# Kernel tuning notes

Measured on AMD Instinct MI355X. Metric: run time of the kernel, lower is better.

Reference implementation:

```python
import jax, jax.numpy as jnp
import numpy as np

N_SIDE = 32          # dense voxel grid side
WINDOW = 8           # window_size
C = 512              # channels
H = 8                # num_heads
D = C // H           # head_dim = 64
EPS = 1e-12          # torch F.normalize eps


def setup_inputs() -> dict:
    key = jax.random.key(0)
    ks = jax.random.split(key, 4)
    N = N_SIDE ** 3
    g = jnp.arange(N_SIDE, dtype=jnp.int32)
    zz, yy, xx = jnp.meshgrid(g, g, g, indexing='ij')
    # coords: [N, 4] = (batch_idx, x, y, z)
    coords = jnp.stack([jnp.zeros((N,), jnp.int32),
                        xx.reshape(-1), yy.reshape(-1), zz.reshape(-1)], axis=-1)
    x_feats = jax.random.normal(ks[0], (N, C), jnp.float32)
    w_qkv = jax.random.normal(ks[1], (C, 3 * C), jnp.float32) / np.sqrt(C).astype(np.float32)
    b_qkv = jnp.zeros((3 * C,), jnp.float32)
    gamma_q = jnp.ones((H, D), jnp.float32)
    gamma_k = jnp.ones((H, D), jnp.float32)
    w_out = jax.random.normal(ks[2], (C, C), jnp.float32) / np.sqrt(C).astype(np.float32)
    b_out = jnp.zeros((C,), jnp.float32)
    return dict(x_feats=x_feats, coords=coords, w_qkv=w_qkv, b_qkv=b_qkv,
                gamma_q=gamma_q, gamma_k=gamma_k, w_out=w_out, b_out=b_out)


def _mh_rms_norm(x, gamma):
    # SparseMultiHeadRMSNorm: L2-normalize last dim, scale by gamma * sqrt(dim)
    xf = x.astype(jnp.float32)
    norm = jnp.maximum(jnp.linalg.norm(xf, axis=-1, keepdims=True), EPS)
    return ((xf / norm) * gamma * np.float32(np.sqrt(D))).astype(x.dtype)


def reference(x_feats, coords, w_qkv, b_qkv, gamma_q, gamma_k, w_out, b_out):
    N = x_feats.shape[0]
    qkv = (x_feats @ w_qkv + b_qkv).reshape(N, 3, H, D)  # [N,3,H,D]
    q = _mh_rms_norm(qkv[:, 0], gamma_q)
    k = _mh_rms_norm(qkv[:, 1], gamma_k)
    v = qkv[:, 2]
    # windowed grouping: window id from voxel coords (shift_window = (0,0,0))
    wc = coords[:, 1:] // WINDOW                       # [N,3]
    nwin = N_SIDE // WINDOW
    wid = (wc[:, 0] * nwin + wc[:, 1]) * nwin + wc[:, 2]
    order = jnp.argsort(wid, stable=True)              # gather points into windows
    inv = jnp.argsort(order)                           # scatter back
    M = WINDOW ** 3                                    # points per window (dense grid)
    W = N // M                                         # number of windows
    qg = q[order].reshape(W, M, H, D)
    kg = k[order].reshape(W, M, H, D)
    vg = v[order].reshape(W, M, H, D)
    scores = jnp.einsum('wmhd,wnhd->whmn', qg, kg) / np.float32(np.sqrt(D))
    attn = jax.nn.softmax(scores, axis=-1)
    hg = jnp.einsum('whmn,wnhd->wmhd', attn, vg)       # [W,M,H,D]
    h = hg.reshape(W * M, H * D)[inv]                  # back to original point order
    return h @ w_out + b_out
```

## Files before the change

### kernel.cpp

```cpp
#include <hip/hip_runtime.h>


typedef __attribute__((ext_vector_type(4))) float f32x4;
typedef __attribute__((ext_vector_type(8))) short s16x8;
typedef __attribute__((ext_vector_type(4))) short s16x4;

#define MFMA(a, b, c) __builtin_amdgcn_mfma_f32_16x16x32_bf16((a), (b), (c), 0, 0, 0)

__device__ __forceinline__ short f2bf(float f) {
  union { float f; unsigned u; } v; v.f = f;
  unsigned r = v.u + 0x7fffu + ((v.u >> 16) & 1u);
  return (short)(r >> 16);
}

__device__ __forceinline__ void gload16(const void* g, void* l) {
  __builtin_amdgcn_global_load_lds(
      (const __attribute__((address_space(1))) unsigned int*)g,
      (__attribute__((address_space(3))) unsigned int*)l, 16, 0, 0);
}

__global__ __launch_bounds__(256) void transpose_w(const float* __restrict__ w,
                                                   short* __restrict__ wt,
                                                   int Ncols) {
  __shared__ float tile[64][65];
  const int t = threadIdx.x;
  const int ntn = Ncols >> 6;
  const int bk = blockIdx.x / ntn, bn = blockIdx.x % ntn;
  const int c = t & 63, r0 = t >> 6;
#pragma unroll
  for (int i = 0; i < 16; ++i) {
    int k = i * 4 + r0;
    tile[k][c] = w[(size_t)(bk * 64 + k) * Ncols + bn * 64 + c];
  }
  __syncthreads();
#pragma unroll
  for (int i = 0; i < 16; ++i) {
    int n = i * 4 + r0;
    wt[(size_t)(bn * 64 + n) * 512 + bk * 64 + c] = f2bf(tile[c][n]);
  }
}

__global__ __launch_bounds__(256) void gather_x(const float* __restrict__ x,
                                                const int* __restrict__ coords,
                                                short* __restrict__ xs,
                                                int* __restrict__ nofp) {
  const int t = threadIdx.x, lane = t & 63, wid = t >> 6;
  const int n = blockIdx.x * 4 + wid;
  const int cx = coords[n * 4 + 1], cy = coords[n * 4 + 2], cz = coords[n * 4 + 3];
  const int w = ((cx >> 3) * 4 + (cy >> 3)) * 4 + (cz >> 3);
  const int r = ((cz & 7) << 6) | ((cy & 7) << 3) | (cx & 7);
  const int p = w * 512 + r;
  const f32x4* xr = (const f32x4*)(x + (size_t)n * 512);
  f32x4 v0 = xr[lane * 2], v1 = xr[lane * 2 + 1];
  s16x8 o;
  o[0] = f2bf(v0[0]); o[1] = f2bf(v0[1]); o[2] = f2bf(v0[2]); o[3] = f2bf(v0[3]);
  o[4] = f2bf(v1[0]); o[5] = f2bf(v1[1]); o[6] = f2bf(v1[2]); o[7] = f2bf(v1[3]);
  *(s16x8*)(xs + (size_t)p * 512 + lane * 8) = o;
  if (lane == 0) nofp[p] = n;
}

__global__ __launch_bounds__(256) void gemm_qkv(
    const short* __restrict__ xs, const short* __restrict__ wt,
    const float* __restrict__ bqkv, const float* __restrict__ gq,
    const float* __restrict__ gk, short* __restrict__ Qs,
    short* __restrict__ Ks, short* __restrict__ Vt) {
  __shared__ short As[128 * 32];
  __shared__ short Bs[128 * 32];
  const int t = threadIdx.x, lane = t & 63, wid = t >> 6;
  const int bm = blockIdx.x / 12, bn = blockIdx.x % 12;
  const int wr = wid >> 1, wc = wid & 1;
  const int rowbase = bm * 128, colbase = bn * 128;
  f32x4 acc[4][4];
#pragma unroll
  for (int m = 0; m < 4; ++m)
#pragma unroll
    for (int n = 0; n < 4; ++n) acc[m][n] = (f32x4){0.f, 0.f, 0.f, 0.f};

  const int srow = lane >> 2, sslot = lane & 3;
  for (int kt = 0; kt < 16; ++kt) {
#pragma unroll
    for (int i = 0; i < 2; ++i) {
      int row = i * 64 + wid * 16 + srow;
      int gc = sslot ^ ((row >> 2) & 3);
      gload16(xs + (size_t)(rowbase + row) * 512 + kt * 32 + gc * 8,
              &As[(i * 64 + wid * 16) * 32]);
      gload16(wt + (size_t)(colbase + row) * 512 + kt * 32 + gc * 8,
              &Bs[(i * 64 + wid * 16) * 32]);
    }
    __syncthreads();
    s16x8 af[4], bfr[4];
#pragma unroll
    for (int m = 0; m < 4; ++m) {
      int row = wr * 64 + m * 16 + (lane & 15);
      int ch = (lane >> 4) ^ ((row >> 2) & 3);
      af[m] = *(const s16x8*)&As[row * 32 + ch * 8];
    }
#pragma unroll
    for (int n = 0; n < 4; ++n) {
      int row = wc * 64 + n * 16 + (lane & 15);
      int ch = (lane >> 4) ^ ((row >> 2) & 3);
      bfr[n] = *(const s16x8*)&Bs[row * 32 + ch * 8];
    }
#pragma unroll
    for (int m = 0; m < 4; ++m)
#pragma unroll
      for (int n = 0; n < 4; ++n) acc[m][n] = MFMA(af[m], bfr[n], acc[m][n]);
    __syncthreads();
  }

  const int wcb = colbase + wc * 64;
  const int which = wcb >> 9;
  const int h = (wcb >> 6) & 7;
  float bias[4], gam[4];
#pragma unroll
  for (int n = 0; n < 4; ++n) {
    int d = n * 16 + (lane & 15);
    bias[n] = bqkv[wcb + d];
    gam[n] = (which == 0) ? gq[h * 64 + d] : (which == 1) ? gk[h * 64 + d] : 1.0f;
  }
#pragma unroll
  for (int m = 0; m < 4; ++m) {
#pragma unroll
    for (int n = 0; n < 4; ++n)
#pragma unroll
      for (int j = 0; j < 4; ++j) acc[m][n][j] += bias[n];
    if (which < 2) {
      float ss[4] = {0.f, 0.f, 0.f, 0.f};
#pragma unroll
      for (int n = 0; n < 4; ++n)
#pragma unroll
        for (int j = 0; j < 4; ++j) ss[j] += acc[m][n][j] * acc[m][n][j];
      float scl[4];
#pragma unroll
      for (int j = 0; j < 4; ++j) {
#pragma unroll
        for (int msk = 1; msk < 16; msk <<= 1) ss[j] += __shfl_xor(ss[j], msk, 64);
        float nrm = fmaxf(sqrtf(ss[j]), 1e-12f);
        scl[j] = ((which == 0) ? 1.0f : 8.0f) / nrm;
      }
#pragma unroll
      for (int j = 0; j < 4; ++j) {
        int p = rowbase + wr * 64 + m * 16 + (lane >> 4) * 4 + j;
        int w = p >> 9, mm = p & 511;
#pragma unroll
        for (int n = 0; n < 4; ++n) {
          int d = n * 16 + (lane & 15);
          float v = acc[m][n][j] * gam[n] * scl[j];
          if (which == 0)
            Qs[((w * 8 + h) * 512 + mm) * 64 + d] = f2bf(v);
          else
            Ks[((w * 8 + h) * 512 + mm) * 64 + d] = f2bf(v);
        }
      }
    } else {
      int pb = rowbase + wr * 64 + m * 16 + (lane >> 4) * 4;
      int w = pb >> 9, mm = pb & 511;
#pragma unroll
      for (int n = 0; n < 4; ++n) {
        int d = n * 16 + (lane & 15);
        s16x4 pk;
#pragma unroll
        for (int j = 0; j < 4; ++j) pk[j] = f2bf(acc[m][n][j]);
        *(s16x4*)&Vt[((size_t)(w * 8 + h) * 64 + d) * 512 + mm] = pk;
      }
    }
  }
}

__global__ __launch_bounds__(256) void attn_k(const short* __restrict__ Qs,
                                              const short* __restrict__ Ks,
                                              const short* __restrict__ Vt,
                                              short* __restrict__ Hs) {
  __shared__ short Pl[4][32 * 64];
  const int t = threadIdx.x, lane = t & 63, wid = t >> 6;
  const int bid = blockIdx.x;
  const int swz = (bid & 7) * 256 + (bid >> 3);
  const int wv = swz * 4 + wid;
  const int wh = wv >> 4;
  const int qt = wv & 15;
  const short* Qb = Qs + (size_t)wh * 512 * 64;
  const short* Kb = Ks + (size_t)wh * 512 * 64;
  const short* Vb = Vt + (size_t)wh * 64 * 512;
  short* slab = Pl[wid];

  s16x8 aq[2][2];
#pragma unroll
  for (int mi = 0; mi < 2; ++mi)
#pragma unroll
    for (int ks = 0; ks < 2; ++ks) {
      int row = qt * 32 + mi * 16 + (lane & 15);
      aq[mi][ks] = *(const s16x8*)&Qb[row * 64 + ks * 32 + (lane >> 4) * 8];
    }
  f32x4 oacc[2][4];
  float rm[2][4], rl[2][4];
#pragma unroll
  for (int mi = 0; mi < 2; ++mi) {
#pragma unroll
    for (int n = 0; n < 4; ++n) oacc[mi][n] = (f32x4){0.f, 0.f, 0.f, 0.f};
#pragma unroll
    for (int j = 0; j < 4; ++j) { rm[mi][j] = -1e30f; rl[mi][j] = 0.f; }
  }

  for (int kt = 0; kt < 8; ++kt) {
    const int kb = kt * 64;
    f32x4 s[2][4];
#pragma unroll
    for (int mi = 0; mi < 2; ++mi)
#pragma unroll
      for (int n = 0; n < 4; ++n) s[mi][n] = (f32x4){0.f, 0.f, 0.f, 0.f};
#pragma unroll
    for (int ks = 0; ks < 2; ++ks)
#pragma unroll
      for (int n = 0; n < 4; ++n) {
        int kr = kb + n * 16 + (lane & 15);
        s16x8 bk = *(const s16x8*)&Kb[kr * 64 + ks * 32 + (lane >> 4) * 8];
        s[0][n] = MFMA(aq[0][ks], bk, s[0][n]);
        s[1][n] = MFMA(aq[1][ks], bk, s[1][n]);
      }

#pragma unroll
    for (int mi = 0; mi < 2; ++mi)
#pragma unroll
      for (int j = 0; j < 4; ++j) {
        float v = fmaxf(fmaxf(s[mi][0][j], s[mi][1][j]),
                        fmaxf(s[mi][2][j], s[mi][3][j]));
#pragma unroll
        for (int msk = 1; msk < 16; msk <<= 1) v = fmaxf(v, __shfl_xor(v, msk, 64));
        if (!__all(v - rm[mi][j] <= 8.0f)) {
          float nm = fmaxf(rm[mi][j], v);
          float f = __expf(rm[mi][j] - nm);
          rm[mi][j] = nm;
          rl[mi][j] *= f;
#pragma unroll
          for (int n2 = 0; n2 < 4; ++n2) oacc[mi][n2][j] *= f;
        }
        float sum = 0.f;
#pragma unroll
        for (int n = 0; n < 4; ++n) {
          float pe = __expf(s[mi][n][j] - rm[mi][j]);
          s[mi][n][j] = pe;
          sum += pe;
        }
#pragma unroll
        for (int msk = 1; msk < 16; msk <<= 1) sum += __shfl_xor(sum, msk, 64);
        rl[mi][j] += sum;
      }

#pragma unroll
    for (int mi = 0; mi < 2; ++mi)
#pragma unroll
      for (int n = 0; n < 4; ++n)
#pragma unroll
        for (int j = 0; j < 4; ++j) {
          int r = mi * 16 + (lane >> 4) * 4 + j;
          int col = n * 16 + (lane & 15);
          slab[r * 64 + (((col >> 3) ^ (r & 7)) << 3) + (col & 7)] =
              f2bf(s[mi][n][j]);
        }

#pragma unroll
    for (int ks = 0; ks < 2; ++ks) {
      s16x8 ap[2];
#pragma unroll
      for (int mi = 0; mi < 2; ++mi) {
        int row = mi * 16 + (lane & 15);
        int ch = (ks * 4 + (lane >> 4)) ^ (row & 7);
        ap[mi] = *(const s16x8*)&slab[row * 64 + ch * 8];
      }
#pragma unroll
      for (int n2 = 0; n2 < 4; ++n2) {
        int dr = n2 * 16 + (lane & 15);
        s16x8 bv = *(const s16x8*)&Vb[dr * 512 + kb + ks * 32 + (lane >> 4) * 8];
        oacc[0][n2] = MFMA(ap[0], bv, oacc[0][n2]);
        oacc[1][n2] = MFMA(ap[1], bv, oacc[1][n2]);
      }
    }
  }

  const int w = wh >> 3, hh = wh & 7;
#pragma unroll
  for (int mi = 0; mi < 2; ++mi)
#pragma unroll
    for (int j = 0; j < 4; ++j) {
      float inv = 1.0f / rl[mi][j];
      int row = qt * 32 + mi * 16 + (lane >> 4) * 4 + j;
      int p = w * 512 + row;
#pragma unroll
      for (int n2 = 0; n2 < 4; ++n2) {
        int d = n2 * 16 + (lane & 15);
        Hs[(size_t)p * 512 + hh * 64 + d] = f2bf(oacc[mi][n2][j] * inv);
      }
    }
}

__global__ __launch_bounds__(256) void gemm_out_k(
    const short* __restrict__ Hs, const short* __restrict__ wt,
    const float* __restrict__ bout, const int* __restrict__ nofp,
    float* __restrict__ out) {
  __shared__ short As[128 * 32];
  __shared__ short Bs[128 * 32];
  const int t = threadIdx.x, lane = t & 63, wid = t >> 6;
  const int bm = blockIdx.x >> 2, bn = blockIdx.x & 3;
  const int wr = wid >> 1, wc = wid & 1;
  const int rowbase = bm * 128, colbase = bn * 128;
  f32x4 acc[4][4];
#pragma unroll
  for (int m = 0; m < 4; ++m)
#pragma unroll
    for (int n = 0; n < 4; ++n) acc[m][n] = (f32x4){0.f, 0.f, 0.f, 0.f};

  const int srow = lane >> 2, sslot = lane & 3;
  for (int kt = 0; kt < 16; ++kt) {
#pragma unroll
    for (int i = 0; i < 2; ++i) {
      int row = i * 64 + wid * 16 + srow;
      int gc = sslot ^ ((row >> 2) & 3);
      gload16(Hs + (size_t)(rowbase + row) * 512 + kt * 32 + gc * 8,
              &As[(i * 64 + wid * 16) * 32]);
      gload16(wt + (size_t)(colbase + row) * 512 + kt * 32 + gc * 8,
              &Bs[(i * 64 + wid * 16) * 32]);
    }
    __syncthreads();
    s16x8 af[4], bfr[4];
#pragma unroll
    for (int m = 0; m < 4; ++m) {
      int row = wr * 64 + m * 16 + (lane & 15);
      int ch = (lane >> 4) ^ ((row >> 2) & 3);
      af[m] = *(const s16x8*)&As[row * 32 + ch * 8];
    }
#pragma unroll
    for (int n = 0; n < 4; ++n) {
      int row = wc * 64 + n * 16 + (lane & 15);
      int ch = (lane >> 4) ^ ((row >> 2) & 3);
      bfr[n] = *(const s16x8*)&Bs[row * 32 + ch * 8];
    }
#pragma unroll
    for (int m = 0; m < 4; ++m)
#pragma unroll
      for (int n = 0; n < 4; ++n) acc[m][n] = MFMA(af[m], bfr[n], acc[m][n]);
    __syncthreads();
  }
#pragma unroll
  for (int m = 0; m < 4; ++m)
#pragma unroll
    for (int j = 0; j < 4; ++j) {
      int p = rowbase + wr * 64 + m * 16 + (lane >> 4) * 4 + j;
      int norig = nofp[p];
#pragma unroll
      for (int n = 0; n < 4; ++n) {
        int c = colbase + wc * 64 + n * 16 + (lane & 15);
        out[(size_t)norig * 512 + c] = acc[m][n][j] + bout[c];
      }
    }
}

extern "C" void kernel_launch(void* const* d_in, const int* in_sizes, int n_in,
                              void* d_out, int out_size, void* d_ws,
                              size_t ws_size, hipStream_t stream) {
  const float* x      = (const float*)d_in[0];
  const int*   coords = (const int*)d_in[1];
  const float* wqkv   = (const float*)d_in[2];
  const float* bqkv   = (const float*)d_in[3];
  const float* gq     = (const float*)d_in[4];
  const float* gk     = (const float*)d_in[5];
  const float* wout   = (const float*)d_in[6];
  const float* bout   = (const float*)d_in[7];
  float* out = (float*)d_out;
  char* ws = (char*)d_ws;

  short* xs    = (short*)(ws + 0);
  short* wqkvt = (short*)(ws + 33554432);
  short* woutt = (short*)(ws + 35127296);
  short* Qs    = (short*)(ws + 35651584);
  short* Ks    = (short*)(ws + 69206016);
  short* Vt    = (short*)(ws + 102760448);
  short* Hs    = (short*)(ws + 136314880);
  int*   nofp  = (int*)(ws + 169869312);

  transpose_w<<<dim3(192), dim3(256), 0, stream>>>(wqkv, wqkvt, 1536);
  transpose_w<<<dim3(64), dim3(256), 0, stream>>>(wout, woutt, 512);
  gather_x<<<dim3(8192), dim3(256), 0, stream>>>(x, coords, xs, nofp);
  gemm_qkv<<<dim3(3072), dim3(256), 0, stream>>>(xs, wqkvt, bqkv, gq, gk, Qs, Ks, Vt);
  attn_k<<<dim3(2048), dim3(256), 0, stream>>>(Qs, Ks, Vt, Hs);
  gemm_out_k<<<dim3(1024), dim3(256), 0, stream>>>(Hs, woutt, bout, nofp, out);
}
```

Baseline: 427.4 us.

## Rewrite windowed attention with transposed 32x32 MFMA and register-resident P

The attention kernel now uses 32x32x16 bf16 MFMA and computes S^T = K·Q^T, so each lane holds one query column's scores. Row max and sum then need only a single cross-half shuffle instead of 16-lane butterfly reductions. P is packed to bf16 with v_cvt_pk and exchanged between lane halves by shuffle, which removes the LDS staging slab for the PV product. This trades LDS traffic and reductions for a larger accumulator footprint, which raises register pressure and may lower occupancy.

```diff
diff --git a/kernel.cpp b/kernel.cpp
--- a/kernel.cpp
+++ b/kernel.cpp
@@ -2,15 +2,24 @@
 
 
 typedef __attribute__((ext_vector_type(4))) float f32x4;
+typedef __attribute__((ext_vector_type(16))) float f32x16;
 typedef __attribute__((ext_vector_type(8))) short s16x8;
 typedef __attribute__((ext_vector_type(4))) short s16x4;
+typedef __attribute__((ext_vector_type(4))) int i32x4;
 
 #define MFMA(a, b, c) __builtin_amdgcn_mfma_f32_16x16x32_bf16((a), (b), (c), 0, 0, 0)
+#define MFMA32(a, b, c) __builtin_amdgcn_mfma_f32_32x32x16_bf16((a), (b), (c), 0, 0, 0)
 
 __device__ __forceinline__ short f2bf(float f) {
   union { float f; unsigned u; } v; v.f = f;
   unsigned r = v.u + 0x7fffu + ((v.u >> 16) & 1u);
   return (short)(r >> 16);
+}
+
+__device__ __forceinline__ int cvtpk(float a, float b) {
+  int r;
+  asm("v_cvt_pk_bf16_f32 %0, %1, %2" : "=v"(r) : "v"(a), "v"(b));
+  return r;
 }
 
 __device__ __forceinline__ void gload16(const void* g, void* l) {
@@ -171,126 +180,101 @@
                                               const short* __restrict__ Ks,
                                               const short* __restrict__ Vt,
                                               short* __restrict__ Hs) {
-  __shared__ short Pl[4][32 * 64];
   const int t = threadIdx.x, lane = t & 63, wid = t >> 6;
+  const int lo = lane & 31, hi = lane >> 5;
   const int bid = blockIdx.x;
   const int swz = (bid & 7) * 256 + (bid >> 3);
   const int wv = swz * 4 + wid;
   const int wh = wv >> 4;
-  const int qt = wv & 15;
+  const int qbase = (wv & 15) * 32;
   const short* Qb = Qs + (size_t)wh * 512 * 64;
   const short* Kb = Ks + (size_t)wh * 512 * 64;
   const short* Vb = Vt + (size_t)wh * 64 * 512;
-  short* slab = Pl[wid];
-
-  s16x8 aq[2][2];
-#pragma unroll
-  for (int mi = 0; mi < 2; ++mi)
-#pragma unroll
-    for (int ks = 0; ks < 2; ++ks) {
-      int row = qt * 32 + mi * 16 + (lane & 15);
-      aq[mi][ks] = *(const s16x8*)&Qb[row * 64 + ks * 32 + (lane >> 4) * 8];
-    }
-  f32x4 oacc[2][4];
-  float rm[2][4], rl[2][4];
-#pragma unroll
-  for (int mi = 0; mi < 2; ++mi) {
-#pragma unroll
-    for (int n = 0; n < 4; ++n) oacc[mi][n] = (f32x4){0.f, 0.f, 0.f, 0.f};
-#pragma unroll
-    for (int j = 0; j < 4; ++j) { rm[mi][j] = -1e30f; rl[mi][j] = 0.f; }
-  }
-
-  for (int kt = 0; kt < 8; ++kt) {
-    const int kb = kt * 64;
-    f32x4 s[2][4];
-#pragma unroll
-    for (int mi = 0; mi < 2; ++mi)
-#pragma unroll
-      for (int n = 0; n < 4; ++n) s[mi][n] = (f32x4){0.f, 0.f, 0.f, 0.f};
-#pragma unroll
-    for (int ks = 0; ks < 2; ++ks)
-#pragma unroll
-      for (int n = 0; n < 4; ++n) {
-        int kr = kb + n * 16 + (lane & 15);
-        s16x8 bk = *(const s16x8*)&Kb[kr * 64 + ks * 32 + (lane >> 4) * 8];
-        s[0][n] = MFMA(aq[0][ks], bk, s[0][n]);
-        s[1][n] = MFMA(aq[1][ks], bk, s[1][n]);
-      }
-
-#pragma unroll
-    for (int mi = 0; mi < 2; ++mi)
-#pragma unroll
-      for (int j = 0; j < 4; ++j) {
-        float v = fmaxf(fmaxf(s[mi][0][j], s[mi][1][j]),
-                        fmaxf(s[mi][2][j], s[mi][3][j]));
-#pragma unroll
-        for (int msk = 1; msk < 16; msk <<= 1) v = fmaxf(v, __shfl_xor(v, msk, 64));
-        if (!__all(v - rm[mi][j] <= 8.0f)) {
-          float nm = fmaxf(rm[mi][j], v);
-          float f = __expf(rm[mi][j] - nm);
-          rm[mi][j] = nm;
-          rl[mi][j] *= f;
-#pragma unroll
-          for (int n2 = 0; n2 < 4; ++n2) oacc[mi][n2][j] *= f;
-        }
-        float sum = 0.f;
-#pragma unroll
-        for (int n = 0; n < 4; ++n) {
-          float pe = __expf(s[mi][n][j] - rm[mi][j]);
-          s[mi][n][j] = pe;
-          sum += pe;
-        }
-#pragma unroll
-        for (int msk = 1; msk < 16; msk <<= 1) sum += __shfl_xor(sum, msk, 64);
-        rl[mi][j] += sum;
-      }
-
-#pragma unroll
-    for (int mi = 0; mi < 2; ++mi)
-#pragma unroll
-      for (int n = 0; n < 4; ++n)
-#pragma unroll
-        for (int j = 0; j < 4; ++j) {
-          int r = mi * 16 + (lane >> 4) * 4 + j;
-          int col = n * 16 + (lane & 15);
-          slab[r * 64 + (((col >> 3) ^ (r & 7)) << 3) + (col & 7)] =
-              f2bf(s[mi][n][j]);
-        }
-
-#pragma unroll
-    for (int ks = 0; ks < 2; ++ks) {
-      s16x8 ap[2];
-#pragma unroll
-      for (int mi = 0; mi < 2; ++mi) {
-        int row = mi * 16 + (lane & 15);
-        int ch = (ks * 4 + (lane >> 4)) ^ (row & 7);
-        ap[mi] = *(const s16x8*)&slab[row * 64 + ch * 8];
-      }
-#pragma unroll
-      for (int n2 = 0; n2 < 4; ++n2) {
-        int dr = n2 * 16 + (lane & 15);
-        s16x8 bv = *(const s16x8*)&Vb[dr * 512 + kb + ks * 32 + (lane >> 4) * 8];
-        oacc[0][n2] = MFMA(ap[0], bv, oacc[0][n2]);
-        oacc[1][n2] = MFMA(ap[1], bv, oacc[1][n2]);
-      }
-    }
-  }
-
+
+  s16x8 qf[4];
+#pragma unroll
+  for (int j = 0; j < 4; ++j)
+    qf[j] = *(const s16x8*)&Qb[(qbase + lo) * 64 + j * 16 + hi * 8];
+
+  f32x16 oacc0, oacc1;
+#pragma unroll
+  for (int c = 0; c < 16; ++c) { oacc0[c] = 0.f; oacc1[c] = 0.f; }
+  float m = -1e30f, l = 0.f;
+
+  for (int kt = 0; kt < 16; ++kt) {
+    const int kb = kt * 32;
+    s16x8 kf0 = *(const s16x8*)&Kb[(kb + lo) * 64 + 0 + hi * 8];
+    s16x8 kf1 = *(const s16x8*)&Kb[(kb + lo) * 64 + 16 + hi * 8];
+    s16x8 kf2 = *(const s16x8*)&Kb[(kb + lo) * 64 + 32 + hi * 8];
+    s16x8 kf3 = *(const s16x8*)&Kb[(kb + lo) * 64 + 48 + hi * 8];
+    f32x16 sc;
+#pragma unroll
+    for (int c = 0; c < 16; ++c) sc[c] = 0.f;
+    sc = MFMA32(kf0, qf[0], sc);
+    sc = MFMA32(kf1, qf[1], sc);
+    sc = MFMA32(kf2, qf[2], sc);
+    sc = MFMA32(kf3, qf[3], sc);
+    s16x8 vf00 = *(const s16x8*)&Vb[(lo)*512 + kb + 0 + hi * 8];
+    s16x8 vf10 = *(const s16x8*)&Vb[(32 + lo) * 512 + kb + 0 + hi * 8];
+    s16x8 vf01 = *(const s16x8*)&Vb[(lo)*512 + kb + 16 + hi * 8];
+    s16x8 vf11 = *(const s16x8*)&Vb[(32 + lo) * 512 + kb + 16 + hi * 8];
+
+    float mx;
+    {
+      float t1 = fmaxf(fmaxf(sc[0], sc[1]), fmaxf(sc[2], sc[3]));
+      float t2 = fmaxf(fmaxf(sc[4], sc[5]), fmaxf(sc[6], sc[7]));
+      float t3 = fmaxf(fmaxf(sc[8], sc[9]), fmaxf(sc[10], sc[11]));
+      float t4 = fmaxf(fmaxf(sc[12], sc[13]), fmaxf(sc[14], sc[15]));
+      mx = fmaxf(fmaxf(t1, t2), fmaxf(t3, t4));
+    }
+    mx = fmaxf(mx, __shfl_xor(mx, 32, 64));
+    if (!__all(mx - m <= 8.0f)) {
+      float nm = fmaxf(m, mx);
+      float f = __expf(m - nm);
+      m = nm; l *= f;
+#pragma unroll
+      for (int c = 0; c < 16; ++c) { oacc0[c] *= f; oacc1[c] *= f; }
+    }
+    float p[16];
+#pragma unroll
+    for (int c = 0; c < 16; ++c) p[c] = __expf(sc[c] - m);
+    float sum = ((p[0] + p[1]) + (p[2] + p[3])) + ((p[4] + p[5]) + (p[6] + p[7])) +
+                (((p[8] + p[9]) + (p[10] + p[11])) + ((p[12] + p[13]) + (p[14] + p[15])));
+    sum += __shfl_xor(sum, 32, 64);
+    l += sum;
+
+    int a0 = cvtpk(p[0], p[1]), a1 = cvtpk(p[2], p[3]);
+    int b0 = cvtpk(p[4], p[5]), b1 = cvtpk(p[6], p[7]);
+    int c0 = cvtpk(p[8], p[9]), c1 = cvtpk(p[10], p[11]);
+    int d0 = cvtpk(p[12], p[13]), d1 = cvtpk(p[14], p[15]);
+    int xa0 = __shfl_xor(a0, 32, 64), xa1 = __shfl_xor(a1, 32, 64);
+    int xb0 = __shfl_xor(b0, 32, 64), xb1 = __shfl_xor(b1, 32, 64);
+    int xc0 = __shfl_xor(c0, 32, 64), xc1 = __shfl_xor(c1, 32, 64);
+    int xd0 = __shfl_xor(d0, 32, 64), xd1 = __shfl_xor(d1, 32, 64);
+    union { i32x4 i; s16x8 s; } f0u, f1u;
+    f0u.i = hi ? (i32x4){xb0, xb1, b0, b1} : (i32x4){a0, a1, xa0, xa1};
+    f1u.i = hi ? (i32x4){xd0, xd1, d0, d1} : (i32x4){c0, c1, xc0, xc1};
+
+    oacc0 = MFMA32(vf00, f0u.s, oacc0);
+    oacc1 = MFMA32(vf10, f0u.s, oacc1);
+    oacc0 = MFMA32(vf01, f1u.s, oacc0);
+    oacc1 = MFMA32(vf11, f1u.s, oacc1);
+  }
+
+  const float inv = 1.0f / l;
   const int w = wh >> 3, hh = wh & 7;
-#pragma unroll
-  for (int mi = 0; mi < 2; ++mi)
+  const size_t prow = (size_t)(w * 512 + qbase + lo) * 512 + hh * 64;
+#pragma unroll
+  for (int g = 0; g < 4; ++g) {
+    s16x4 o0, o1;
 #pragma unroll
     for (int j = 0; j < 4; ++j) {
-      float inv = 1.0f / rl[mi][j];
-      int row = qt * 32 + mi * 16 + (lane >> 4) * 4 + j;
-      int p = w * 512 + row;
-#pragma unroll
-      for (int n2 = 0; n2 < 4; ++n2) {
-        int d = n2 * 16 + (lane & 15);
-        Hs[(size_t)p * 512 + hh * 64 + d] = f2bf(oacc[mi][n2][j] * inv);
-      }
-    }
+      o0[j] = f2bf(oacc0[g * 4 + j] * inv);
+      o1[j] = f2bf(oacc1[g * 4 + j] * inv);
+    }
+    *(s16x4*)&Hs[prow + g * 8 + hi * 4] = o0;
+    *(s16x4*)&Hs[prow + 32 + g * 8 + hi * 4] = o1;
+  }
 }
 
 __global__ __launch_bounds__(256) void gemm_out_k(
```

Result: faster. 379.0 us (-11.3%).
